# Performance work log

Hardware: AMD Instinct MI355X
Metric: run time of the kernel (lower is better)

Reference implementation:

```python
import jax, jax.numpy as jnp
import numpy as np

CONF_THRES = 0.25
IOU_THRES = 0.45
K = 1000          # fixed candidate count after confidence filter (pad/mask form of NMS)
MAX_WH = 4096.0   # class offset for class-aware (batched) NMS, as in yolov5


def _xywh2xyxy(b):
    cx, cy, w, h = b[..., 0], b[..., 1], b[..., 2], b[..., 3]
    return jnp.stack([cx - w * 0.5, cy - h * 0.5, cx + w * 0.5, cy + h * 0.5], axis=-1)


def _box_iou(a, b):
    # a: [K,4], b: [K,4] in xyxy -> [K,K] IoU
    area_a = (a[:, 2] - a[:, 0]) * (a[:, 3] - a[:, 1])
    area_b = (b[:, 2] - b[:, 0]) * (b[:, 3] - b[:, 1])
    lt = jnp.maximum(a[:, None, :2], b[None, :, :2])
    rb = jnp.minimum(a[:, None, 2:], b[None, :, 2:])
    wh = jnp.clip(rb - lt, 0.0)
    inter = wh[..., 0] * wh[..., 1]
    return inter / (area_a[:, None] + area_b[None, :] - inter + 1e-7)


def _nms_single(pred):
    # pred: [N, 5+C] = [cx,cy,w,h,obj, cls...]
    obj = pred[:, 4]
    cls_conf = obj[:, None] * pred[:, 5:]            # conf = obj * cls (yolov5)
    best = jnp.max(cls_conf, axis=-1)                # best-class score per box
    j = jnp.argmax(cls_conf, axis=-1)                # best class index
    valid = (obj > CONF_THRES) & (best > CONF_THRES)  # candidate + confidence filter
    score = jnp.where(valid, best, 0.0)

    vals, idx = jax.lax.top_k(score, K)              # descending -> greedy NMS order
    boxes = _xywh2xyxy(pred[:, :4])[idx]             # [K,4]
    cls = j[idx].astype(pred.dtype)                  # [K]

    off_boxes = boxes + (cls * MAX_WH)[:, None]      # class-aware offset
    iou = _box_iou(off_boxes, off_boxes)             # [K,K]

    ar = jnp.arange(K)

    def body(keep, inp):
        i, row = inp
        ki = keep[i]
        sup = (row > IOU_THRES) & (ar > i) & (ki > 0.5)
        return jnp.where(sup, 0.0, keep), None

    keep, _ = jax.lax.scan(body, jnp.ones((K,), pred.dtype), (ar, iou))

    final_score = vals * keep * (vals > CONF_THRES).astype(pred.dtype)
    # [K,6]: x1,y1,x2,y2,score,class ; suppressed/padded rows have score==0
    return jnp.concatenate([boxes, final_score[:, None], cls[:, None]], axis=-1)


def setup_inputs() -> dict:
    key = jax.random.key(0)
    B, N, C = 16, 25200, 85
    k1, k2 = jax.random.split(key)
    # plausible 640x640 detections: centers in [0,640), w/h in (0,100)
    xywh = jax.random.uniform(k1, (B, N, 4), dtype=jnp.float32) * jnp.array(
        [640.0, 640.0, 100.0, 100.0], dtype=jnp.float32)
    scores = jax.random.uniform(k2, (B, N, C - 4), dtype=jnp.float32)  # obj + 80 cls
    x = jnp.concatenate([xywh, scores], axis=-1)
    return {"x": x}


def reference(x):
    return jax.vmap(_nms_single)(x)  # [B, K, 6]
```

## Files before the change

kernel.cpp:

```cpp
#include <hip/hip_runtime.h>
#include <stdint.h>

#define BB 16
#define NN 25200
#define CC 85
#define NCLS 80
#define KK 1000
#define CAP 2048
#define NBIN 4096
#define BINBASE 0x3E800000u
#define TILE 84
#define NTILE 300
#define SBLK 384
#define CTILE 25
#define CNTSTRIDE 64
#define MBLK 40
#define RBLK 32
#define CONF 0.25f
#define IOUT 0.45f
#define MAXWH 4096.0f
#define NW 16
#define CHUNK 96

#define STG_FULL 27648
#define STG_TAIL4 57
#define STG_FULL4 1728

#define AS1(p) ((const __attribute__((address_space(1))) void*)(p))
#define AS3(p) ((__attribute__((address_space(3))) void*)(p))

typedef unsigned long long u64;
typedef unsigned int u32;

__device__ __forceinline__ u64 umax64(u64 a, u64 b) { return a > b ? a : b; }

__device__ __forceinline__ u32 score_bin(u32 sb) {
  u32 d = (sb - BINBASE) >> 12;
  return d > (NBIN - 1) ? (NBIN - 1) : d;
}

__global__ __launch_bounds__(256) void k_zero(uint4* __restrict__ p, int n4) {
  int i = blockIdx.x * 256 + threadIdx.x;
  if (i < n4) p[i] = make_uint4(0u, 0u, 0u, 0u);
}

__global__ __launch_bounds__(SBLK) void k_score(const float* __restrict__ x,
                                                u64* __restrict__ keys,
                                                u32* __restrict__ hist) {
#pragma clang fp contract(off)
  __shared__ float tile[TILE * CC];
  __shared__ u32 zc;
  int b = blockIdx.x / NTILE;
  int t = blockIdx.x % NTILE;
  int tid = threadIdx.x;
  int base_row = t * TILE;
  const char* gb = (const char*)(x + ((size_t)b * NN + base_row) * CC);
  const float4* src4 = (const float4*)gb;
  float4* tile4 = (float4*)tile;
  if (tid == 0) zc = 0;

  int wv = tid >> 6, ln = tid & 63;
  for (int off = wv * 1024; off < STG_FULL; off += 6 * 1024) {
    __builtin_amdgcn_global_load_lds(AS1(gb + off + ln * 16),
                                     AS3((char*)tile + off), 16, 0, 0);
  }
  if (tid < STG_TAIL4) tile4[STG_FULL4 + tid] = src4[STG_FULL4 + tid];
  __syncthreads();

  if (tid < TILE * 4) {
    int row = tid >> 2, r = tid & 3;
    const float* rp = tile + row * CC;
    float obj = rp[4];
    float best = -1.0f;
    int bj = 0;
#pragma unroll
    for (int c = 0; c < 20; ++c) {
      float p = obj * rp[5 + r * 20 + c];
      if (p > best) { best = p; bj = r * 20 + c; }
    }
    u64 ck = ((u64)__float_as_uint(best) << 32) | (u32)(~(u32)bj);
    ck = umax64(ck, __shfl_xor(ck, 1));
    ck = umax64(ck, __shfl_xor(ck, 2));
    if (r == 0) {
      float bestv = __uint_as_float((u32)(ck >> 32));
      u32 j = ~(u32)(ck & 0xFFFFFFFFu);
      bool valid = (obj > CONF) && (bestv > CONF);
      float score = valid ? bestv : 0.0f;
      u32 sb = __float_as_uint(score);
      int n = base_row + row;
      u64 key = ((u64)sb << 32) | ((u64)(~(u32)n & 0xFFFFu) << 16) |
                ((u64)(j & 0xFFu) << 8);
      keys[(size_t)b * NN + n] = key;
      if (sb) {
        atomicAdd(&hist[b * NBIN + score_bin(sb)], 1u);
      } else {
        atomicAdd(&zc, 1u);
      }
    }
  }
  __syncthreads();
  if (tid == 0 && zc) atomicAdd(&hist[b * NBIN + 0], zc);
}

__global__ __launch_bounds__(1024) void k_pivot(const u32* __restrict__ hist,
                                                u32* __restrict__ pinfo) {
  __shared__ u32 s[1024];
  int b = blockIdx.x, tid = threadIdx.x;
  const uint4* h4 = (const uint4*)(hist + b * NBIN);
  uint4 v = h4[tid];
  u32 c = v.x + v.y + v.z + v.w;
  s[tid] = c;
  __syncthreads();
  u32 inc = c;
  for (int off = 1; off < 1024; off <<= 1) {
    u32 add = (tid + off < 1024) ? s[tid + off] : 0u;
    __syncthreads();
    inc += add;
    s[tid] = inc;
    __syncthreads();
  }
  if (inc >= KK && inc - c < KK) {
    u32 cum = inc - c;
    u32 hv[4] = {v.x, v.y, v.z, v.w};
    for (int i = 3; i >= 0; --i) {
      u32 hh = hv[i];
      if (cum + hh >= KK) { pinfo[b] = (u32)(tid * 4 + i); break; }
      cum += hh;
    }
  }
}

__global__ __launch_bounds__(1024) void k_compact2(const u64* __restrict__ keys,
                                                   const u32* __restrict__ pinfo,
                                                   u64* __restrict__ cand,
                                                   u32* __restrict__ cnt) {
  int b = blockIdx.x / CTILE;
  int t = blockIdx.x % CTILE;
  int tid = threadIdx.x;
  u32 pivot = pinfo[b];

  int n = t * 1024 + tid;
  bool cond = false;
  u64 key = 0;
  if (n < NN) {
    key = keys[(size_t)b * NN + n];
    u32 sb = (u32)(key >> 32);
    cond = sb && (score_bin(sb) >= pivot);
  }
  u64 m = __ballot(cond);
  if (!m) return;
  int lane = tid & 63;
  u32 prefix = (u32)__popcll(m & ((1ULL << lane) - 1ULL));
  u32 tot = (u32)__popcll(m);
  int leader = (int)__ffsll((long long)m) - 1;
  u32 base = 0;
  if (lane == leader) base = atomicAdd(&cnt[b * CNTSTRIDE], tot);
  base = (u32)__shfl((int)base, leader);
  if (cond) {
    u32 pos = base + prefix;
    if (pos < CAP) cand[(size_t)b * CAP + pos] = key;
  }
}

__global__ __launch_bounds__(256) void k_rank(const float* __restrict__ x,
                                              const u64* __restrict__ cand,
                                              const u32* __restrict__ cnt,
                                              float* __restrict__ out,
                                              float* __restrict__ offbox,
                                              float* __restrict__ vals) {
#pragma clang fp contract(off)
  __shared__ u64 lbuf[CAP];
  __shared__ u32 part[4][64];
  int b = blockIdx.x / RBLK;
  int chunk = blockIdx.x % RBLK;
  int tid = threadIdx.x;
  for (int i = tid; i < CAP; i += 256)
    lbuf[i] = cand[(size_t)b * CAP + i];
  __syncthreads();
  u32 total = cnt[b * CNTSTRIDE];
  if (total > CAP) total = CAP;

  int c = tid & 63;
  int seg = tid >> 6;
  int ci = chunk * 64 + c;
  u64 k = lbuf[ci];
  u32 pc = 0;
  if (k != 0ULL) {
    int j = seg;
#pragma unroll 4
    for (; j < (int)total; j += 4) pc += (lbuf[j] > k);
  }
  part[seg][c] = pc;
  __syncthreads();
  if (seg != 0) return;
  if (k == 0ULL) return;
  u32 rank = part[0][c] + part[1][c] + part[2][c] + part[3][c];
  if (rank >= KK) return;

  u32 ni = 65535u - (u32)((k >> 16) & 0xFFFFu);
  if (ni > NN - 1) ni = NN - 1;
  u32 cj = (u32)((k >> 8) & 0xFFu);
  float val = __uint_as_float((u32)(k >> 32));
  const float* row = x + ((size_t)b * NN + ni) * CC;
  float cx = row[0], cy = row[1], w = row[2], h = row[3];
  float x1 = cx - w * 0.5f, y1 = cy - h * 0.5f;
  float x2 = cx + w * 0.5f, y2 = cy + h * 0.5f;
  float cls = (float)cj;
  float off = cls * MAXWH;
  float* o = out + ((size_t)b * KK + rank) * 6;
  o[0] = x1; o[1] = y1; o[2] = x2; o[3] = y2; o[5] = cls;
  float* ob = offbox + ((size_t)b * KK + rank) * 4;
  ob[0] = x1 + off; ob[1] = y1 + off; ob[2] = x2 + off; ob[3] = y2 + off;
  vals[(size_t)b * KK + rank] = val;
}

__global__ __launch_bounds__(256) void k_mask(const float* __restrict__ offbox,
                                              u64* __restrict__ mask,
                                              u64* __restrict__ rowflag) {
#pragma clang fp contract(off)
  __shared__ float jx1[64], jy1[64], jx2[64], jy2[64], jar[64];
  int tid = threadIdx.x;
  int blk = blockIdx.x;
  int b = blk / MBLK;
  int s = blk % MBLK;
  int w = 0, r0 = 0;
  for (int g = 0; g < 16; ++g) {
    int nb = (g >> 2) + 1;
    if (s < nb) { w = g; r0 = s * 256; break; }
    s -= nb;
  }
  const float4* ob4 = (const float4*)(offbox + (size_t)b * KK * 4);
  if (tid < 64) {
    int j = w * 64 + tid;
    float4 v = (j < KK) ? ob4[j] : make_float4(0.f, 0.f, 0.f, 0.f);
    jx1[tid] = v.x; jy1[tid] = v.y; jx2[tid] = v.z; jy2[tid] = v.w;
    jar[tid] = (v.z - v.x) * (v.w - v.y);
  }
  __syncthreads();
  int i = r0 + tid;
  int rows_w = KK < 64 * (w + 1) ? KK : 64 * (w + 1);
  if (i >= rows_w) return;
  float4 A = ob4[i];
  float aa = (A.z - A.x) * (A.w - A.y);
  u64 bits = 0ULL;
  int j0 = w * 64;
#pragma unroll 4
  for (int jj = 0; jj < 64; ++jj) {
    int j = j0 + jj;
    if (j <= i) continue;
    float lx = fmaxf(A.x, jx1[jj]), ly = fmaxf(A.y, jy1[jj]);
    float rx = fminf(A.z, jx2[jj]), ry = fminf(A.w, jy2[jj]);
    float ww = rx - lx; ww = ww > 0.0f ? ww : 0.0f;
    float hh = ry - ly; hh = hh > 0.0f ? hh : 0.0f;
    float inter = ww * hh;
    float denom = aa + jar[jj] - inter + 1e-7f;
    if (inter > IOUT * denom) bits |= (1ULL << jj);
  }
  mask[((size_t)b * KK + i) * NW + w] = bits;
  if (bits)
    atomicOr(&rowflag[(size_t)b * NW + (i >> 6)], 1ULL << (i & 63));
}

__global__ __launch_bounds__(64) void k_scan(const u64* __restrict__ mask,
                                             const u64* __restrict__ rowflag,
                                             const float* __restrict__ vals,
                                             float* __restrict__ out) {
  int b = blockIdx.x;
  int lane = threadIdx.x;
  int w = lane & 15;
  const u64* mb = mask + (size_t)b * KK * NW;
  __shared__ int rows[CHUNK];
  __shared__ u64 mrow[CHUNK][NW];
  __shared__ u64 skeep[NW];
  __shared__ int s_n;
  u64 keep = ~0ULL;

  u64 f0 = 0;
  int W0 = 0;
  if (lane == 0) f0 = rowflag[(size_t)b * NW + 0];

  while (true) {
    if (lane == 0) {
      int n = 0;
      while (n < CHUNK) {
        while (W0 < NW && f0 == 0ULL) {
          W0++;
          if (W0 < NW) f0 = rowflag[(size_t)b * NW + W0];
        }
        if (W0 >= NW) break;
        int bit = (int)__ffsll((long long)f0) - 1;
        f0 &= f0 - 1ULL;
        rows[n++] = W0 * 64 + bit;
      }
      s_n = n;
    }
    __syncthreads();
    int n = s_n;
    if (n > 0) {
      for (int r = lane >> 4; r < n; r += 4) {
        int word = lane & 15;
        u64 v = mb[(size_t)rows[r] * NW + word];
        mrow[r][word] = (word < (rows[r] >> 6)) ? 0ULL : v;
      }
      __syncthreads();
      for (int idx = 0; idx < n; ++idx) {
        int i_ = rows[idx];
        int wi_ = i_ >> 6;
        u32 half_ = (i_ & 32) ? (u32)(keep >> 32) : (u32)keep;
        u32 kw_ = (u32)__builtin_amdgcn_readlane((int)half_, wi_);
        u32 bit_ = (kw_ >> (i_ & 31)) & 1u;
        keep &= bit_ ? ~mrow[idx][w] : ~0ULL;
      }
      __syncthreads();
    }
    if (n < CHUNK) break;
  }

  if (lane < NW) skeep[lane] = keep;
  __syncthreads();
  for (int s2 = lane; s2 < KK; s2 += 64) {
    float v = vals[(size_t)b * KK + s2];
    u64 kwv = skeep[s2 >> 6];
    float kbit = (float)((kwv >> (s2 & 63)) & 1ULL);
    float fs = v * kbit * (v > CONF ? 1.0f : 0.0f);
    out[((size_t)b * KK + s2) * 6 + 4] = fs;
  }
}

extern "C" void kernel_launch(void* const* d_in, const int* in_sizes, int n_in,
                              void* d_out, int out_size, void* d_ws,
                              size_t ws_size, hipStream_t stream) {
  const float* x = (const float*)d_in[0];
  float* out = (float*)d_out;
  char* ws = (char*)d_ws;
  (void)in_sizes; (void)n_in; (void)out_size; (void)ws_size;

  auto align256 = [](size_t v) { return (v + 255) & ~(size_t)255; };
  size_t keys_off = 0;
  size_t keys_sz = (size_t)BB * NN * 8;
  size_t hist_off = align256(keys_off + keys_sz);
  size_t hist_sz = (size_t)BB * NBIN * 4;
  size_t cand_off = hist_off + hist_sz;
  size_t cand_sz = (size_t)BB * CAP * 8;
  size_t cnt_off = cand_off + cand_sz;
  size_t cnt_sz = (size_t)BB * CNTSTRIDE * 4;
  size_t rowflag_off = cnt_off + cnt_sz;
  size_t rowflag_sz = (size_t)BB * NW * 8;
  size_t pinfo_off = rowflag_off + rowflag_sz;
  size_t pinfo_sz = 256;
  size_t zero_sz = hist_sz + cand_sz + cnt_sz + rowflag_sz + pinfo_sz;
  size_t offbox_off = align256(pinfo_off + pinfo_sz);
  size_t offbox_sz = (size_t)BB * KK * 4 * 4;
  size_t vals_off = align256(offbox_off + offbox_sz);
  size_t vals_sz = (size_t)BB * KK * 4;
  size_t mask_off = align256(vals_off + vals_sz);
  size_t mask_sz = (size_t)BB * KK * NW * 8;
  (void)mask_sz;

  u64* keys = (u64*)(ws + keys_off);
  u32* hist = (u32*)(ws + hist_off);
  u64* cand = (u64*)(ws + cand_off);
  u32* cnt = (u32*)(ws + cnt_off);
  u64* rowflag = (u64*)(ws + rowflag_off);
  u32* pinfo = (u32*)(ws + pinfo_off);
  float* offbox = (float*)(ws + offbox_off);
  float* vals = (float*)(ws + vals_off);
  u64* mask = (u64*)(ws + mask_off);

  int n4 = (int)(zero_sz / 16);
  k_zero<<<dim3((n4 + 255) / 256), dim3(256), 0, stream>>>(
      (uint4*)(ws + hist_off), n4);
  k_score<<<dim3(BB * NTILE), dim3(SBLK), 0, stream>>>(x, keys, hist);
  k_pivot<<<dim3(BB), dim3(1024), 0, stream>>>(hist, pinfo);
  k_compact2<<<dim3(BB * CTILE), dim3(1024), 0, stream>>>(keys, pinfo, cand,
                                                          cnt);
  k_rank<<<dim3(BB * RBLK), dim3(256), 0, stream>>>(x, cand, cnt, out, offbox,
                                                    vals);
  k_mask<<<dim3(BB * MBLK), dim3(256), 0, stream>>>(offbox, mask, rowflag);
  k_scan<<<dim3(BB), dim3(64), 0, stream>>>(mask, rowflag, vals, out);
}
```

Measured before the change: 75.71 us.

## Skip cross-class IoU pairs via per-class bitmasks; widen rank kernel to 512 threads

k_rank now writes each candidate's class index to a new workspace buffer, and k_mask builds a shared per-class 64-bit mask of the column tile. Each row then iterates only over same-class columns with ffs instead of testing all 64 columns. Boxes of different classes can never overlap because of the class offset, so this cuts IoU work by roughly the class count. k_rank also moves to 512 threads (8 segments) so the counting loop runs at higher parallelism, at the cost of an extra global buffer, shared atomics and divergent while-loops.

```diff
diff --git a/kernel.cpp b/kernel.cpp
--- a/kernel.cpp
+++ b/kernel.cpp
@@ -162,19 +162,20 @@
   }
 }
 
-__global__ __launch_bounds__(256) void k_rank(const float* __restrict__ x,
+__global__ __launch_bounds__(512) void k_rank(const float* __restrict__ x,
                                               const u64* __restrict__ cand,
                                               const u32* __restrict__ cnt,
                                               float* __restrict__ out,
                                               float* __restrict__ offbox,
-                                              float* __restrict__ vals) {
+                                              float* __restrict__ vals,
+                                              u32* __restrict__ clsb) {
 #pragma clang fp contract(off)
   __shared__ u64 lbuf[CAP];
-  __shared__ u32 part[4][64];
+  __shared__ u32 part[8][64];
   int b = blockIdx.x / RBLK;
   int chunk = blockIdx.x % RBLK;
   int tid = threadIdx.x;
-  for (int i = tid; i < CAP; i += 256)
+  for (int i = tid; i < CAP; i += 512)
     lbuf[i] = cand[(size_t)b * CAP + i];
   __syncthreads();
   u32 total = cnt[b * CNTSTRIDE];
@@ -188,13 +189,14 @@
   if (k != 0ULL) {
     int j = seg;
 #pragma unroll 4
-    for (; j < (int)total; j += 4) pc += (lbuf[j] > k);
+    for (; j < (int)total; j += 8) pc += (lbuf[j] > k);
   }
   part[seg][c] = pc;
   __syncthreads();
   if (seg != 0) return;
   if (k == 0ULL) return;
-  u32 rank = part[0][c] + part[1][c] + part[2][c] + part[3][c];
+  u32 rank = part[0][c] + part[1][c] + part[2][c] + part[3][c] +
+             part[4][c] + part[5][c] + part[6][c] + part[7][c];
   if (rank >= KK) return;
 
   u32 ni = 65535u - (u32)((k >> 16) & 0xFFFFu);
@@ -212,13 +214,16 @@
   float* ob = offbox + ((size_t)b * KK + rank) * 4;
   ob[0] = x1 + off; ob[1] = y1 + off; ob[2] = x2 + off; ob[3] = y2 + off;
   vals[(size_t)b * KK + rank] = val;
+  clsb[(size_t)b * KK + rank] = cj;
 }
 
 __global__ __launch_bounds__(256) void k_mask(const float* __restrict__ offbox,
+                                              const u32* __restrict__ clsb,
                                               u64* __restrict__ mask,
                                               u64* __restrict__ rowflag) {
 #pragma clang fp contract(off)
   __shared__ float jx1[64], jy1[64], jx2[64], jy2[64], jar[64];
+  __shared__ u64 clsmask[NCLS];
   int tid = threadIdx.x;
   int blk = blockIdx.x;
   int b = blk / MBLK;
@@ -230,11 +235,17 @@
     s -= nb;
   }
   const float4* ob4 = (const float4*)(offbox + (size_t)b * KK * 4);
+  if (tid < NCLS) clsmask[tid] = 0ULL;
+  __syncthreads();
   if (tid < 64) {
     int j = w * 64 + tid;
     float4 v = (j < KK) ? ob4[j] : make_float4(0.f, 0.f, 0.f, 0.f);
     jx1[tid] = v.x; jy1[tid] = v.y; jx2[tid] = v.z; jy2[tid] = v.w;
     jar[tid] = (v.z - v.x) * (v.w - v.y);
+    if (j < KK) {
+      u32 cj = clsb[(size_t)b * KK + j] & (NCLS - 1);
+      atomicOr(&clsmask[cj], 1ULL << tid);
+    }
   }
   __syncthreads();
   int i = r0 + tid;
@@ -242,12 +253,16 @@
   if (i >= rows_w) return;
   float4 A = ob4[i];
   float aa = (A.z - A.x) * (A.w - A.y);
+  u32 ci = clsb[(size_t)b * KK + i] & (NCLS - 1);
+  u64 cand = clsmask[ci];
+  if ((i >> 6) == w) {
+    int sh = (i & 63) + 1;
+    cand = (sh == 64) ? 0ULL : (cand & (~0ULL << sh));
+  }
   u64 bits = 0ULL;
-  int j0 = w * 64;
-#pragma unroll 4
-  for (int jj = 0; jj < 64; ++jj) {
-    int j = j0 + jj;
-    if (j <= i) continue;
+  while (cand) {
+    int jj = (int)__ffsll((long long)cand) - 1;
+    cand &= cand - 1ULL;
     float lx = fmaxf(A.x, jx1[jj]), ly = fmaxf(A.y, jy1[jj]);
     float rx = fminf(A.z, jx2[jj]), ry = fminf(A.w, jy2[jj]);
     float ww = rx - lx; ww = ww > 0.0f ? ww : 0.0f;
@@ -353,7 +368,9 @@
   size_t offbox_sz = (size_t)BB * KK * 4 * 4;
   size_t vals_off = align256(offbox_off + offbox_sz);
   size_t vals_sz = (size_t)BB * KK * 4;
-  size_t mask_off = align256(vals_off + vals_sz);
+  size_t clsb_off = align256(vals_off + vals_sz);
+  size_t clsb_sz = (size_t)BB * KK * 4;
+  size_t mask_off = align256(clsb_off + clsb_sz);
   size_t mask_sz = (size_t)BB * KK * NW * 8;
   (void)mask_sz;
 
@@ -365,6 +382,7 @@
   u32* pinfo = (u32*)(ws + pinfo_off);
   float* offbox = (float*)(ws + offbox_off);
   float* vals = (float*)(ws + vals_off);
+  u32* clsb = (u32*)(ws + clsb_off);
   u64* mask = (u64*)(ws + mask_off);
 
   int n4 = (int)(zero_sz / 16);
@@ -374,8 +392,9 @@
   k_pivot<<<dim3(BB), dim3(1024), 0, stream>>>(hist, pinfo);
   k_compact2<<<dim3(BB * CTILE), dim3(1024), 0, stream>>>(keys, pinfo, cand,
                                                           cnt);
-  k_rank<<<dim3(BB * RBLK), dim3(256), 0, stream>>>(x, cand, cnt, out, offbox,
-                                                    vals);
-  k_mask<<<dim3(BB * MBLK), dim3(256), 0, stream>>>(offbox, mask, rowflag);
+  k_rank<<<dim3(BB * RBLK), dim3(512), 0, stream>>>(x, cand, cnt, out, offbox,
+                                                    vals, clsb);
+  k_mask<<<dim3(BB * MBLK), dim3(256), 0, stream>>>(offbox, clsb, mask,
+                                                    rowflag);
   k_scan<<<dim3(BB), dim3(64), 0, stream>>>(mask, rowflag, vals, out);
 }
```

Result: faster. 67.61 us (-10.7%).
